# Optimization experiments

Hardware: AMD Instinct MI355X
Metric: run time of the kernel (lower is better)

Reference implementation:

```python
import jax, jax.numpy as jnp
import numpy as np

R = 2                                   # NMS radius (init kwarg r)
EPS = float(np.finfo(np.float32).eps)   # torch.finfo(float32).eps
PI = float(np.pi)


def _sobel(x):
    """Kornia SpatialGradient (sobel, normalized): x [N,1,H,W] -> (dx, dy) each [N,1,H,W]."""
    kx = jnp.array([[-1., 0., 1.], [-2., 0., 2.], [-1., 0., 1.]], jnp.float32) / 8.0
    ky = kx.T
    k = jnp.stack([kx, ky])[:, None]    # [2,1,3,3] -> out channels dx, dy
    xp = jnp.pad(x, ((0, 0), (0, 0), (1, 1), (1, 1)), mode='edge')  # replicate pad
    out = jax.lax.conv_general_dilated(xp, k, (1, 1), 'VALID',
                                       dimension_numbers=('NCHW', 'OIHW', 'NCHW'))
    return out[:, 0:1], out[:, 1:2]


def _theta(mask):
    """Edge direction from one-hot mask, per STEAL edges_nms. mask [N,1,H,W]."""
    dx, dy = _sobel(mask)
    gxx, _ = _sobel(dx)
    gxy, gyy = _sobel(dy)
    return jnp.fmod(jnp.arctan(gyy * jnp.sign(-gxy + EPS) / (gxx + EPS)), PI)


def setup_inputs() -> dict:
    key = jax.random.key(0)
    k1, k2 = jax.random.split(key)
    pred_labels = jax.random.normal(k1, (4, 16, 512, 1024), dtype=jnp.float32)
    true_labels = jax.random.randint(k2, (4, 512, 1024), 0, 16, dtype=jnp.int64)
    return {"pred_labels": pred_labels, "true_labels": true_labels}


def reference(pred_labels, true_labels):
    B, C, H, W = pred_labels.shape
    # per-class one-hot masks -> direction maps
    onehot = jax.nn.one_hot(true_labels, C, dtype=jnp.float32)        # [B,H,W,C]
    masks = onehot.transpose(0, 3, 1, 2).reshape(B * C, 1, H, W)
    theta = _theta(masks).reshape(B, C, H, W)
    thresh_theta = jnp.fmod(jnp.round(theta * (5.0 / PI)) + 5.0, 5.0)  # {0..4}
    dirs = jnp.fmod(thresh_theta, 4.0).astype(jnp.int32)               # {0,1,2,3}

    exp_p = jnp.exp(pred_labels)
    js = list(range(-R, R))
    # offsets (dx_off, dy_off) summed in the denominator for each direction
    offs = {
        0: [(0, j) for j in js],        # horizontal: preds[x, y-r:y+r]
        1: [(j, -j - 1) for j in js],   # anti-diagonal
        2: [(j, 0) for j in js],        # vertical: preds[x-r:x+r, y]
        3: [(-j - 1, j) for j in js],   # anti-diagonal (reversed traversal, same set)
    }
    denom = jnp.ones_like(exp_p)
    for d in range(4):
        dd = exp_p * 0.0
        for ox, oy in offs[d]:
            dd = dd + jnp.roll(exp_p, (-ox, -oy), axis=(2, 3))  # exp_p[x+ox, y+oy]
        denom = jnp.where(dirs == d, dd, denom)

    interior = jnp.zeros((H, W), bool).at[R:H - R, R:W - R].set(True)
    nms = jnp.where(interior, exp_p / denom, 0.0)
    return jnp.sum(nms)
```

## Files before the change

### kernel.cpp

```cpp
#include <hip/hip_runtime.h>


#define Bn 4
#define Cn 16
#define Hn 512
#define Wn 1024

typedef unsigned long long u64;
typedef unsigned int u32;
typedef float f4u __attribute__((ext_vector_type(4), aligned(4)));
typedef int   i4u __attribute__((ext_vector_type(4), aligned(4)));

static __device__ __forceinline__ float fast_rcp(float x) {
#if __has_builtin(__builtin_amdgcn_rcpf)
  return __builtin_amdgcn_rcpf(x);
#else
  return 1.0f / x;
#endif
}


#define P1TW 128
#define P1TH 8
#define P1LW 132
#define P1LH 12

__global__ __launch_bounds__(256)
void dir_kernel(const int* __restrict__ labels, u32* __restrict__ dirs)
{
  __shared__ unsigned char labt[P1LH][P1LW];

  const int w0 = blockIdx.x * P1TW;
  const int h0 = blockIdx.y * P1TH;
  const int b  = blockIdx.z;
  const int tid = threadIdx.x;

  const int* lbase = labels + (size_t)b * (Hn*Wn);
  const bool interior = (h0 >= 2) && (h0 + P1TH + 2 <= Hn) &&
                        (w0 >= 2) && (w0 + P1TW + 2 <= Wn);
  if (interior) {
    const int* lb = lbase + (size_t)(h0-2)*Wn + (w0-2);
    for (int i = tid; i < P1LH*33; i += 256) {
      int row = i / 33, c4 = (i - row*33) * 4;
      i4u L = *(const i4u*)(lb + row*Wn + c4);
      *(u32*)&labt[row][c4] =
          (u32)L.x | ((u32)L.y << 8) | ((u32)L.z << 16) | ((u32)L.w << 24);
    }
  } else {
    for (int i = tid; i < P1LH*33; i += 256) {
      int row = i / 33, c4 = (i - row*33) * 4;
      int gh = min(max(h0-2+row, 0), Hn-1);
      const int* lr = lbase + gh*Wn;
      u32 v = 0;
      #pragma unroll
      for (int k = 0; k < 4; ++k) {
        int gw = min(max(w0-2+c4+k, 0), Wn-1);
        v |= (u32)(lr[gw] & 0xff) << (8*k);
      }
      *(u32*)&labt[row][c4] = v;
    }
  }
  __syncthreads();

  const int tcol = tid & 31;
  const int trow = tid >> 5;

  u64 W[5];
  #pragma unroll
  for (int r = 0; r < 5; ++r) {
    const u32* lp = (const u32*)&labt[trow + r][0];
    u64 lo = lp[tcol];
    u64 hi = lp[tcol + 1];
    W[r] = lo | (hi << 32);
  }

  u32 pack[4] = {0u, 0u, 0u, 0u};

  #pragma unroll 1
  for (int c = 0; c < 16; ++c) {
    const u64 crep = 0x0101010101010101ULL * (u32)c;
    u64 m[5];
    #pragma unroll
    for (int r = 0; r < 5; ++r) {
      u64 x = W[r] ^ crep;
      m[r] = ((0x8080808080808080ULL - x) & 0x8080808080808080ULL) >> 7;
    }
    u64 t  = m[1] + m[3];
    u64 VA = m[0] + m[4] + (t << 2) + (m[2] << 2) + (m[2] << 1);
    u64 VB = ((m[3] << 1) + m[4] + 0x0303030303030303ULL)
             - (m[0] + (m[1] << 1));
    u64 VC = (m[0] + m[4] + 0x0202020202020202ULL) - (m[2] << 1);
    u64 gxxp = (VA + (VA >> 32) + 0x4040404040404040ULL) - ((VA >> 16) << 1);
    u64 q1   = (VC >> 8) + (VC >> 24);
    u64 w16  = VC >> 16;
    u64 gyyp = (VC + (VC >> 32)) + (q1 << 2) + (w16 << 2) + (w16 << 1);
    u64 gxyp = (((VB >> 24) << 1) + (VB >> 32) + 0x2020202020202020ULL)
             - (VB + ((VB >> 8) << 1));

    u32 gxxl = (u32)gxxp, gyyl = (u32)gyyp, gxyl = (u32)gxyp;
    #pragma unroll
    for (int k = 0; k < 4; ++k) {
      int gxx = (int)((gxxl >> (8*k)) & 0xffu) - 64;
      int gyy = (int)((gyyl >> (8*k)) & 0xffu) - 32;
      int gxyb = (int)((gxyl >> (8*k)) & 0xffu);
      int ax = gxx < 0 ? -gxx : gxx;
      int ay = gyy < 0 ? -gyy : gyy;
      int t1 = (__mul24(ay, 100)  > __mul24(ax, 33))   ? 1 : 0;
      int t2 = (__mul24(ay, 1000) > __mul24(ax, 1377)) ? 1 : 0;
      int rb = t1 + t2;
      bool ng = ((gyy < 0) != (gxyb > 32)) != (gxx < 0);
      int dir = ng ? ((rb == 2) ? 3 : 0) : rb;
      pack[k] |= (u32)dir << (2*c);
    }
  }

  const int gh = h0 + trow;
  u32* drow = dirs + ((size_t)b*Hn + gh)*Wn + (w0 + 4*tcol);
  *(uint4*)drow = make_uint4(pack[0], pack[1], pack[2], pack[3]);
}


#define TW 128
#define TH 32
#define LW 132
#define LH 36
#define NT 256

__global__ __launch_bounds__(NT)
void nms_sum_kernel(const float* __restrict__ pred,
                    const u32* __restrict__ dirs,
                    float* __restrict__ slots)
{
  __shared__ float ext[LH*LW];
  __shared__ float wsum[NT/64];

  const int w0 = blockIdx.x * TW;
  const int h0 = blockIdx.y * TH;
  const int bz = blockIdx.z;
  const int b  = bz >> 4;
  const int c  = bz & 15;
  const int tid = threadIdx.x;

  const int x  = tid & 127;
  const int rg = tid >> 7;
  const int gw = w0 + x;

  const u32* dbase = dirs + (size_t)b*Hn*Wn + (size_t)(h0 + rg*16)*Wn + gw;
  u32 dv[16];
  #pragma unroll
  for (int r = 0; r < 16; ++r) dv[r] = dbase[(size_t)r*Wn];

  const float* plane = pred + (size_t)(b*Cn + c) * (size_t)(Hn*Wn);
  const bool interior = (h0 >= 2) && (h0 + TH + 2 <= Hn) &&
                        (w0 >= 2) && (w0 + TW + 2 <= Wn);
  if (interior) {
    const float* pb = plane + (size_t)(h0-2)*Wn + (w0-2);
    for (int i = tid; i < LH*33; i += NT) {
      int row = i / 33, c4 = (i - row*33) * 4;
      f4u p = *(const f4u*)(pb + row*Wn + c4);
      float4 e;
      e.x = __expf(p.x); e.y = __expf(p.y); e.z = __expf(p.z); e.w = __expf(p.w);
      *(float4*)&ext[row*LW + c4] = e;
    }
  } else {
    for (int i = tid; i < LH*(LW/2); i += NT) {
      int row = i / (LW/2);
      int col = (i - row*(LW/2)) * 2;
      int gh = min(max(h0-2+row, 0), Hn-1);
      int ga = min(max(w0-2+col,   0), Wn-1);
      int gb = min(max(w0-1+col,   0), Wn-1);
      const float* prow = plane + gh*Wn;
      *(float2*)&ext[row*LW+col] = make_float2(__expf(prow[ga]), __expf(prow[gb]));
    }
  }
  __syncthreads();

  const bool wv = (gw >= 2) && (gw < Wn-2);
  const u32 sh = 2u * (u32)c;
  const int ghb = h0 + rg*16;

  float acc = 0.f;
  const int abase = (rg*16 + 2)*LW + (x + 2);

  #pragma unroll
  for (int r = 0; r < 16; ++r) {
    const int a0 = abase + r*LW;
    const int dir = (int)((dv[r] >> sh) & 3u);

    const int o0 = (dir == 0) ? -2 : ((dir == 2) ? -264 : -263);
    const int o1 = (dir == 0) ? -1 : -132;
    const int o2 = -(dir & 1);
    const int o3 = (dir == 0) ?  1 : ((dir == 2) ?  132 :  130);

    float g0 = ext[a0 + o0];
    float g1 = ext[a0 + o1];
    float g2 = ext[a0 + o2];
    float g3 = ext[a0 + o3];
    float num = ext[a0];
    float den = ((g0 + g1) + g2) + g3;

    const int gh = ghb + r;
    const bool hv = (gh >= 2) && (gh < Hn-2);
    float nn = (hv && wv) ? num : 0.f;
    acc += nn * fast_rcp(den);
  }

  const int lane = tid & 63;
  const int wq   = tid >> 6;
  #pragma unroll
  for (int off = 32; off > 0; off >>= 1)
    acc += __shfl_down(acc, off);
  if (lane == 0) wsum[wq] = acc;
  __syncthreads();
  if (tid == 0) {
    float s = 0.f;
    #pragma unroll
    for (int q = 0; q < NT/64; ++q) s += wsum[q];
    atomicAdd(&slots[(bz << 2) | (blockIdx.x & 3)], s);
  }
}

__global__ __launch_bounds__(64)
void reduce_ws_kernel(const float* __restrict__ slots, float* __restrict__ out)
{
  const int l = threadIdx.x;
  float s = (slots[l] + slots[l + 64]) + (slots[l + 128] + slots[l + 192]);
  #pragma unroll
  for (int off = 32; off > 0; off >>= 1)
    s += __shfl_down(s, off);
  if (l == 0) *out = s;
}

extern "C" void kernel_launch(void* const* d_in, const int* in_sizes, int n_in,
                              void* d_out, int out_size, void* d_ws, size_t ws_size,
                              hipStream_t stream) {
  (void)in_sizes; (void)n_in; (void)ws_size; (void)out_size;
  const float* pred   = (const float*)d_in[0];
  const int*   labels = (const int*)d_in[1];
  float* out = (float*)d_out;

  u32*   dirs  = (u32*)d_ws;
  float* slots = (float*)((char*)d_ws + (size_t)Bn*Hn*Wn*sizeof(u32));

  hipMemsetAsync(slots, 0, 256 * sizeof(float), stream);

  dir_kernel<<<dim3(Wn/P1TW, Hn/P1TH, Bn), 256, 0, stream>>>(labels, dirs);
  nms_sum_kernel<<<dim3(Wn/TW, Hn/TH, Bn*Cn), NT, 0, stream>>>(pred, dirs, slots);
  reduce_ws_kernel<<<1, 64, 0, stream>>>(slots, out);
}
```

Baseline: 247.3 us.

## Replace LDS-tiled NMS with register-streaming rows and DPP lane shifts

```diff
diff --git a/kernel.cpp b/kernel.cpp
--- a/kernel.cpp
+++ b/kernel.cpp
@@ -19,6 +19,23 @@
 #endif
 }
 
+static __device__ __forceinline__ float lane_up1(float x) {
+#if __has_builtin(__builtin_amdgcn_update_dpp)
+  return __int_as_float(__builtin_amdgcn_update_dpp(
+      __float_as_int(x), __float_as_int(x), 0x138, 0xF, 0xF, false));
+#else
+  return __shfl_up(x, 1);
+#endif
+}
+static __device__ __forceinline__ float lane_dn1(float x) {
+#if __has_builtin(__builtin_amdgcn_update_dpp)
+  return __int_as_float(__builtin_amdgcn_update_dpp(
+      __float_as_int(x), __float_as_int(x), 0x130, 0xF, 0xF, false));
+#else
+  return __shfl_down(x, 1);
+#endif
+}
+
 
 #define P1TW 128
 #define P1TH 8
@@ -26,7 +43,7 @@
 #define P1LH 12
 
 __global__ __launch_bounds__(256)
-void dir_kernel(const int* __restrict__ labels, u32* __restrict__ dirs)
+void dir_kernel(const int* __restrict__ labels, u32* __restrict__ dirs8w)
 {
   __shared__ unsigned char labt[P1LH][P1LW];
 
@@ -115,109 +132,93 @@
   }
 
   const int gh = h0 + trow;
-  u32* drow = dirs + ((size_t)b*Hn + gh)*Wn + (w0 + 4*tcol);
-  *(uint4*)drow = make_uint4(pack[0], pack[1], pack[2], pack[3]);
-}
-
-
-#define TW 128
-#define TH 32
-#define LW 132
-#define LH 36
-#define NT 256
-
-__global__ __launch_bounds__(NT)
+  const size_t base = (size_t)gh*Wn + (w0 + 4*tcol);
+  #pragma unroll
+  for (int g = 0; g < 4; ++g) {
+    u32 v =  ((pack[0] >> (8*g)) & 0xffu)
+          | (((pack[1] >> (8*g)) & 0xffu) << 8)
+          | (((pack[2] >> (8*g)) & 0xffu) << 16)
+          | (((pack[3] >> (8*g)) & 0xffu) << 24);
+    dirs8w[(((size_t)(g*Bn + b))*(Hn*Wn) + base) >> 2] = v;
+  }
+}
+
+
+__global__ __launch_bounds__(256)
 void nms_sum_kernel(const float* __restrict__ pred,
-                    const u32* __restrict__ dirs,
+                    const unsigned char* __restrict__ dirs8,
                     float* __restrict__ slots)
 {
-  __shared__ float ext[LH*LW];
-  __shared__ float wsum[NT/64];
-
-  const int w0 = blockIdx.x * TW;
-  const int h0 = blockIdx.y * TH;
-  const int bz = blockIdx.z;
-  const int b  = bz >> 4;
-  const int c  = bz & 15;
-  const int tid = threadIdx.x;
-
-  const int x  = tid & 127;
-  const int rg = tid >> 7;
-  const int gw = w0 + x;
-
-  const u32* dbase = dirs + (size_t)b*Hn*Wn + (size_t)(h0 + rg*16)*Wn + gw;
-  u32 dv[16];
-  #pragma unroll
-  for (int r = 0; r < 16; ++r) dv[r] = dbase[(size_t)r*Wn];
-
-  const float* plane = pred + (size_t)(b*Cn + c) * (size_t)(Hn*Wn);
-  const bool interior = (h0 >= 2) && (h0 + TH + 2 <= Hn) &&
-                        (w0 >= 2) && (w0 + TW + 2 <= Wn);
-  if (interior) {
-    const float* pb = plane + (size_t)(h0-2)*Wn + (w0-2);
-    for (int i = tid; i < LH*33; i += NT) {
-      int row = i / 33, c4 = (i - row*33) * 4;
-      f4u p = *(const f4u*)(pb + row*Wn + c4);
-      float4 e;
-      e.x = __expf(p.x); e.y = __expf(p.y); e.z = __expf(p.z); e.w = __expf(p.w);
-      *(float4*)&ext[row*LW + c4] = e;
-    }
-  } else {
-    for (int i = tid; i < LH*(LW/2); i += NT) {
-      int row = i / (LW/2);
-      int col = (i - row*(LW/2)) * 2;
-      int gh = min(max(h0-2+row, 0), Hn-1);
-      int ga = min(max(w0-2+col,   0), Wn-1);
-      int gb = min(max(w0-1+col,   0), Wn-1);
-      const float* prow = plane + gh*Wn;
-      *(float2*)&ext[row*LW+col] = make_float2(__expf(prow[ga]), __expf(prow[gb]));
-    }
-  }
-  __syncthreads();
-
-  const bool wv = (gw >= 2) && (gw < Wn-2);
-  const u32 sh = 2u * (u32)c;
-  const int ghb = h0 + rg*16;
+  const int lane = threadIdx.x & 63;
+  const int wq   = threadIdx.x >> 6;
+  const int s    = blockIdx.x;
+  const int chunk = blockIdx.y * 4 + wq;
+  const int zg   = blockIdx.z;
+  const int b    = zg & 3;
+  const int g    = zg >> 2;
+
+  const int col = 60*s + lane;
+  const int r0  = 32*chunk;
+
+  const float* pl[4];
+  #pragma unroll
+  for (int k = 0; k < 4; ++k)
+    pl[k] = pred + (size_t)(b*Cn + 4*g + k)*(size_t)(Hn*Wn) + col;
+  const unsigned char* dp = dirs8 + (size_t)(g*Bn + b)*(size_t)(Hn*Wn) + col;
+
+  const float wvf = (lane >= 2 && lane < 62) ? 1.f : 0.f;
+
+  float w[4][4];
+  {
+    const int rm2 = max(r0-2, 0), rm1 = max(r0-1, 0);
+    #pragma unroll
+    for (int k = 0; k < 4; ++k) {
+      w[k][2] = __expf(pl[k][(size_t)rm2*Wn]);
+      w[k][3] = __expf(pl[k][(size_t)rm1*Wn]);
+      w[k][0] = __expf(pl[k][(size_t)r0 *Wn]);
+    }
+  }
 
   float acc = 0.f;
-  const int abase = (rg*16 + 2)*LW + (x + 2);
-
-  #pragma unroll
-  for (int r = 0; r < 16; ++r) {
-    const int a0 = abase + r*LW;
-    const int dir = (int)((dv[r] >> sh) & 3u);
-
-    const int o0 = (dir == 0) ? -2 : ((dir == 2) ? -264 : -263);
-    const int o1 = (dir == 0) ? -1 : -132;
-    const int o2 = -(dir & 1);
-    const int o3 = (dir == 0) ?  1 : ((dir == 2) ?  132 :  130);
-
-    float g0 = ext[a0 + o0];
-    float g1 = ext[a0 + o1];
-    float g2 = ext[a0 + o2];
-    float g3 = ext[a0 + o3];
-    float num = ext[a0];
-    float den = ((g0 + g1) + g2) + g3;
-
-    const int gh = ghb + r;
-    const bool hv = (gh >= 2) && (gh < Hn-2);
-    float nn = (hv && wv) ? num : 0.f;
-    acc += nn * fast_rcp(den);
-  }
-
-  const int lane = tid & 63;
-  const int wq   = tid >> 6;
+
+  #pragma unroll 1
+  for (int i8 = 0; i8 < 8; ++i8) {
+    #pragma unroll
+    for (int kk = 0; kk < 4; ++kk) {
+      const int r  = r0 + i8*4 + kk;
+      const int rp = min(r+1, Hn-1);
+      const u32 db = dp[(size_t)r*Wn];
+      const float nmask = ((u32)(r-2) < (u32)(Hn-4)) ? wvf : 0.f;
+
+      #pragma unroll
+      for (int k = 0; k < 4; ++k) {
+        float ne = __expf(pl[k][(size_t)rp*Wn]);
+        w[k][(kk+1)&3] = ne;
+        const float e0 = w[k][(kk+2)&3];
+        const float e1 = w[k][(kk+3)&3];
+        const float e2 = w[k][ kk     ];
+        const float e3 = ne;
+
+        float d  = lane_dn1(e2);
+        float u  = e2 + d;
+        float H  = lane_up1(lane_up1(u)) + u;
+        float V  = ((e0 + e1) + e2) + e3;
+        float p  = lane_dn1(e0);
+        float t  = e2 + lane_up1(e3);
+        float D  = (p + e1) + lane_up1(t);
+
+        int dir = (int)((db >> (2*k)) & 3u);
+        float den = (dir == 0) ? H : ((dir == 2) ? V : D);
+        acc = fmaf(nmask * e2, fast_rcp(den), acc);
+      }
+    }
+  }
+
   #pragma unroll
   for (int off = 32; off > 0; off >>= 1)
     acc += __shfl_down(acc, off);
-  if (lane == 0) wsum[wq] = acc;
-  __syncthreads();
-  if (tid == 0) {
-    float s = 0.f;
-    #pragma unroll
-    for (int q = 0; q < NT/64; ++q) s += wsum[q];
-    atomicAdd(&slots[(bz << 2) | (blockIdx.x & 3)], s);
-  }
+  if (lane == 0)
+    atomicAdd(&slots[(zg << 4) | ((s + chunk) & 15)], acc);
 }
 
 __global__ __launch_bounds__(64)
@@ -239,12 +240,13 @@
   const int*   labels = (const int*)d_in[1];
   float* out = (float*)d_out;
 
-  u32*   dirs  = (u32*)d_ws;
-  float* slots = (float*)((char*)d_ws + (size_t)Bn*Hn*Wn*sizeof(u32));
+  u32* dirs8w = (u32*)d_ws;
+  const unsigned char* dirs8 = (const unsigned char*)d_ws;
+  float* slots = (float*)((char*)d_ws + (size_t)4*Bn*Hn*Wn);
 
   hipMemsetAsync(slots, 0, 256 * sizeof(float), stream);
 
-  dir_kernel<<<dim3(Wn/P1TW, Hn/P1TH, Bn), 256, 0, stream>>>(labels, dirs);
-  nms_sum_kernel<<<dim3(Wn/TW, Hn/TH, Bn*Cn), NT, 0, stream>>>(pred, dirs, slots);
+  dir_kernel<<<dim3(Wn/P1TW, Hn/P1TH, Bn), 256, 0, stream>>>(labels, dirs8w);
+  nms_sum_kernel<<<dim3(17, 4, 16), 256, 0, stream>>>(pred, dirs8, slots);
   reduce_ws_kernel<<<1, 64, 0, stream>>>(slots, out);
 }
```

Measured after the change: 286.3 us. 15.8% more time.
